# Performance work log

Measured on AMD Instinct MI355X. Metric: run time of the kernel, lower is better.

The kernel has to match this reference:

```python
import jax, jax.numpy as jnp
import numpy as np

_EPS = 1e-6
_ZCA_EPS = 1e-5
NEG_SLOPE_ATTN = 0.2   # LeakyReLU inside score_mlp
NEG_SLOPE_FFN = 0.1    # VNLinearLeakyReLU negative_slope


def _safe_norm(x, axis, keepdims=False):
    # norm with zero-gradient at exactly-zero vectors (matches torch subgradient)
    sq = jnp.sum(x * x, axis=axis, keepdims=keepdims)
    safe = jnp.where(sq == 0, 1.0, sq)
    return jnp.sqrt(safe) * (sq > 0)


def vn_linear(W, x):
    # W: (out, in); x: (B, C_in, 3, N) -> (B, C_out, 3, N)
    return jnp.einsum('oi,bivn->bovn', W, x)


def zca_layernorm(x, gamma):
    # x: (B, C, 3, N); whiten the 3D vector components per batch element
    B, C = x.shape[0], x.shape[1]
    xf = x.reshape(B, C, 3, -1).transpose(0, 2, 1, 3).reshape(B, 3, -1)
    xf = xf.astype(jnp.float32)
    mu = xf.mean(axis=-1, keepdims=True)
    xc = xf - mu
    M = xc.shape[-1]
    cov = (xc @ xc.transpose(0, 2, 1)) / (float(M) + _EPS)  # (B,3,3)
    cov = cov + _ZCA_EPS * jnp.eye(3, dtype=cov.dtype)[None]
    w, V = jnp.linalg.eigh(cov)
    w = jnp.maximum(w, _ZCA_EPS)
    Wm = (V * jax.lax.rsqrt(w)[:, None, :]) @ V.transpose(0, 2, 1)  # (B,3,3)
    xw = Wm @ xc
    xw = xw.reshape(B, 3, C, -1).transpose(0, 2, 1, 3).reshape(x.shape).astype(x.dtype)
    return xw * gamma[None, :, None, None]


def cwsa_attention(x, pos, Wq, Wk, Wv, Wo, W1, b1, W2, b2):
    q = vn_linear(Wq, x)  # (B,C,3,N)
    k = vn_linear(Wk, x)
    v = vn_linear(Wv, x)
    qk = q.transpose(0, 3, 1, 2)  # (B,N,C,3)
    kk = k.transpose(0, 3, 1, 2)
    vv = v.transpose(0, 3, 1, 2)
    rel = qk[:, :, None, :, :] - kk[:, None, :, :, :]      # (B,N,N,C,3)
    rel_norm = _safe_norm(rel, axis=-1)                    # (B,N,N,C)
    rel_mean = rel_norm.mean(axis=-1, keepdims=True)       # (B,N,N,1)
    rel_pos = pos[:, :, None, :] - pos[:, None, :, :]      # (B,N,N,3)
    rel_pos_norm = _safe_norm(rel_pos, axis=-1, keepdims=True)  # (B,N,N,1)
    score_in = jnp.concatenate([rel_mean, rel_pos_norm], axis=-1)  # (B,N,N,2)
    h = jax.nn.leaky_relu(score_in @ W1.T + b1, NEG_SLOPE_ATTN)
    scores = h @ W2.T + b2                                  # (B,N,N,C)
    attn = jax.nn.softmax(scores, axis=2)                   # softmax over keys j
    out = jnp.einsum('bijk,bjkd->bikd', attn, vv)           # (B,N,C,3)
    out = out.transpose(0, 2, 3, 1)                         # (B,C,3,N)
    return vn_linear(Wo, out)


def vn_leaky_relu(p, d, ns):
    # p, d: (B, C, 3, N)
    dot = jnp.sum(p * d, axis=2, keepdims=True)
    dsq = jnp.sum(d * d, axis=2, keepdims=True)
    mask = (dot >= 0).astype(p.dtype)
    proj = p - (dot / (dsq + _EPS)) * d
    return ns * p + (1.0 - ns) * (mask * p + (1.0 - mask) * proj)


def ffn(x, Wfeat, Wdir, Wffn2):
    p = vn_linear(Wfeat, x)
    d = vn_linear(Wdir, x)
    h = vn_leaky_relu(p, d, NEG_SLOPE_FFN)
    return vn_linear(Wffn2, h)


def setup_inputs() -> dict:
    key = jax.random.key(0)
    ks = jax.random.split(key, 16)
    B, C, N = 2, 128, 256
    hidden, ratio = 64, 2
    sC = 1.0 / np.sqrt(C)
    inp = {
        'x': jax.random.normal(ks[0], (B, C, 3, N), dtype=jnp.float32),
        'pos': jax.random.normal(ks[1], (B, N, 3), dtype=jnp.float32),
        'Wq': jax.random.normal(ks[2], (C, C), dtype=jnp.float32) * sC,
        'Wk': jax.random.normal(ks[3], (C, C), dtype=jnp.float32) * sC,
        'Wv': jax.random.normal(ks[4], (C, C), dtype=jnp.float32) * sC,
        'Wo': jax.random.normal(ks[5], (C, C), dtype=jnp.float32) * sC,
        'W1': jax.random.normal(ks[6], (hidden, 2), dtype=jnp.float32) * (1.0 / np.sqrt(2.0)),
        'b1': jnp.zeros((hidden,), dtype=jnp.float32),
        'W2': jax.random.normal(ks[7], (C, hidden), dtype=jnp.float32) * (1.0 / np.sqrt(hidden)),
        'b2': jnp.zeros((C,), dtype=jnp.float32),
        'gamma1': jnp.ones((C,), dtype=jnp.float32),
        'Wfeat': jax.random.normal(ks[8], (C * ratio, C), dtype=jnp.float32) * sC,
        'Wdir': jax.random.normal(ks[9], (C * ratio, C), dtype=jnp.float32) * sC,
        'Wffn2': jax.random.normal(ks[10], (C, C * ratio), dtype=jnp.float32) * (1.0 / np.sqrt(C * ratio)),
        'gamma2': jnp.ones((C,), dtype=jnp.float32),
    }
    return inp


def reference(x, pos, Wq, Wk, Wv, Wo, W1, b1, W2, b2, gamma1, Wfeat, Wdir, Wffn2, gamma2):
    a = cwsa_attention(x, pos, Wq, Wk, Wv, Wo, W1, b1, W2, b2)
    x1 = zca_layernorm(x + a, gamma1)
    f = ffn(x1, Wfeat, Wdir, Wffn2)
    return zca_layernorm(x1 + f, gamma2)
```

## Files before the change

### kernel.cpp

```cpp
#include <hip/hip_runtime.h>
#include <math.h>

#define BB 2
#define CC 128
#define NN 256
#define HH 64
#define CHX 256
#define COLS 768
#define NEG_ATTN 0.2f
#define NEG_FFN 0.1f

typedef __attribute__((ext_vector_type(8))) short short8b;
typedef __attribute__((ext_vector_type(4))) float f32x4;

__device__ __forceinline__ unsigned bf16rne(float x) {
  unsigned u = __float_as_uint(x);
  return (u + 0x7fffu + ((u >> 16) & 1u)) >> 16;
}

__global__ __launch_bounds__(256) void k_qkv(
    const float* __restrict__ x, const float* __restrict__ Wq,
    const float* __restrict__ Wk, const float* __restrict__ Wv,
    float* __restrict__ q_t, float* __restrict__ k_nat, float* __restrict__ v_t3)
{
  const int ct = blockIdx.x, which = blockIdx.y, b = blockIdx.z;
  const int col0 = ct * 16;
  __shared__ float xt[CC][16];
  const float* xb = x + (size_t)b * CC * COLS;
  for (int idx = threadIdx.x; idx < CC * 16; idx += 256) {
    int r = idx >> 4, cc = idx & 15;
    xt[r][cc] = xb[r * COLS + col0 + cc];
  }
  __syncthreads();
  const float* W = (which == 0) ? Wq : ((which == 1) ? Wk : Wv);
  const int co = threadIdx.x >> 1;
  const int cc0 = (threadIdx.x & 1) * 8;
  float acc[8];
#pragma unroll
  for (int k = 0; k < 8; k++) acc[k] = 0.f;
  const float* wrow = W + co * CC;
  for (int ci = 0; ci < CC; ci++) {
    float wv = wrow[ci];
#pragma unroll
    for (int k = 0; k < 8; k++) acc[k] = fmaf(wv, xt[ci][cc0 + k], acc[k]);
  }
#pragma unroll
  for (int k = 0; k < 8; k++) {
    int col = col0 + cc0 + k;
    int v = col >> 8, n = col & 255;
    float val = acc[k];
    if (which == 0)      q_t[((size_t)(b * NN + n) * CC + co) * 3 + v] = val;
    else if (which == 1) k_nat[(size_t)(b * CC + co) * COLS + col] = val;
    else                 v_t3[((size_t)(b * NN + n) * CC + co) * 3 + v] = val;
  }
}

__global__ __launch_bounds__(256) void k_rel(
    const float* __restrict__ q_t, const float* __restrict__ k_nat,
    const float* __restrict__ pos, float* __restrict__ rm_all,
    float* __restrict__ rp_all)
{
  const int i = blockIdx.x, b = blockIdx.y;
  const int t = threadIdx.x;
  __shared__ float qv[CC * 3];
  for (int idx = t; idx < CC * 3; idx += 256)
    qv[idx] = q_t[(size_t)(b * NN + i) * CC * 3 + idx];
  __syncthreads();
  const int j = t;
  const float* kb = k_nat + (size_t)b * CC * COLS;
  float p0 = 0.f, p1 = 0.f, p2 = 0.f, p3 = 0.f;
  for (int c = 0; c < CC; c += 4) {
    float kx0 = kb[(c + 0) * COLS + j], ky0 = kb[(c + 0) * COLS + 256 + j], kz0 = kb[(c + 0) * COLS + 512 + j];
    float kx1 = kb[(c + 1) * COLS + j], ky1 = kb[(c + 1) * COLS + 256 + j], kz1 = kb[(c + 1) * COLS + 512 + j];
    float kx2 = kb[(c + 2) * COLS + j], ky2 = kb[(c + 2) * COLS + 256 + j], kz2 = kb[(c + 2) * COLS + 512 + j];
    float kx3 = kb[(c + 3) * COLS + j], ky3 = kb[(c + 3) * COLS + 256 + j], kz3 = kb[(c + 3) * COLS + 512 + j];
    float dx, dy, dz, sq;
    dx = kx0 - qv[(c + 0) * 3]; dy = ky0 - qv[(c + 0) * 3 + 1]; dz = kz0 - qv[(c + 0) * 3 + 2];
    sq = dx * dx + dy * dy + dz * dz; p0 += (sq > 0.f) ? sqrtf(sq) : 0.f;
    dx = kx1 - qv[(c + 1) * 3]; dy = ky1 - qv[(c + 1) * 3 + 1]; dz = kz1 - qv[(c + 1) * 3 + 2];
    sq = dx * dx + dy * dy + dz * dz; p1 += (sq > 0.f) ? sqrtf(sq) : 0.f;
    dx = kx2 - qv[(c + 2) * 3]; dy = ky2 - qv[(c + 2) * 3 + 1]; dz = kz2 - qv[(c + 2) * 3 + 2];
    sq = dx * dx + dy * dy + dz * dz; p2 += (sq > 0.f) ? sqrtf(sq) : 0.f;
    dx = kx3 - qv[(c + 3) * 3]; dy = ky3 - qv[(c + 3) * 3 + 1]; dz = kz3 - qv[(c + 3) * 3 + 2];
    sq = dx * dx + dy * dy + dz * dz; p3 += (sq > 0.f) ? sqrtf(sq) : 0.f;
  }
  rm_all[(size_t)(b * NN + i) * NN + j] = ((p0 + p1) + (p2 + p3)) * (1.f / 128.f);
  float dx = pos[(b * NN + i) * 3 + 0] - pos[(b * NN + j) * 3 + 0];
  float dy = pos[(b * NN + i) * 3 + 1] - pos[(b * NN + j) * 3 + 1];
  float dz = pos[(b * NN + i) * 3 + 2] - pos[(b * NN + j) * 3 + 2];
  float sq = dx * dx + dy * dy + dz * dz;
  rp_all[(size_t)(b * NN + i) * NN + j] = (sq > 0.f) ? sqrtf(sq) : 0.f;
}

__global__ __launch_bounds__(256, 4) void k_attn(
    const float* __restrict__ rm_all, const float* __restrict__ rp_all,
    const float* __restrict__ v_t3, const float* __restrict__ W1,
    const float* __restrict__ b1, const float* __restrict__ W2,
    float* __restrict__ a_nat)
{
  const int i = blockIdx.x, chalf = blockIdx.y, b = blockIdx.z;
  const int t = threadIdx.x;
  __shared__ __align__(16) short hh_s[64 * 64];
  __shared__ __align__(16) short w2_s[64 * 64];
  __shared__ float sc_s[64 * 65];
  __shared__ float rm_s[NN], rp_s[NN];

  rm_s[t] = rm_all[(size_t)(b * NN + i) * NN + t];
  rp_s[t] = rp_all[(size_t)(b * NN + i) * NN + t];
  {
    const int cl = t >> 2, h0 = (t & 3) * 16;
    const float* wrow = W2 + (size_t)(chalf * 64 + cl) * HH + h0;
#pragma unroll
    for (int e = 0; e < 8; e++) {
      unsigned lo = bf16rne(wrow[2 * e]);
      unsigned hi = bf16rne(wrow[2 * e + 1]);
      int didx = (cl * 32 + (h0 >> 1) + e) ^ ((cl & 7) << 2);
      ((unsigned*)w2_s)[didx] = lo | (hi << 16);
    }
  }
  const int h2 = (t & 31) * 2, jgrp = t >> 5;
  const float4 w1v = *reinterpret_cast<const float4*>(W1 + 2 * h2);
  const float c0 = b1[h2], c1 = b1[h2 + 1];
  __syncthreads();

  auto phase2 = [&](int q) {
#pragma unroll
    for (int jj = 0; jj < 8; jj++) {
      int jl = jgrp * 8 + jj;
      int jg = q * 64 + jl;
      float rmv = rm_s[jg], rpv = rp_s[jg];
      float g0 = fmaf(w1v.x, rmv, fmaf(w1v.y, rpv, c0));
      float g1 = fmaf(w1v.z, rmv, fmaf(w1v.w, rpv, c1));
      g0 = (g0 >= 0.f) ? g0 : NEG_ATTN * g0;
      g1 = (g1 >= 0.f) ? g1 : NEG_ATTN * g1;
      int didx = (jl * 32 + (h2 >> 1)) ^ ((jl & 7) << 2);
      ((unsigned*)hh_s)[didx] = bf16rne(g0) | (bf16rne(g1) << 16);
    }
  };

  phase2(0);
  __syncthreads();

  const int lane = t & 63, wv = t >> 6;
  const int g8 = (lane >> 4) * 8;
  const int cdx = wv * 16 + (lane & 15);
  const short8b bfr0 = *reinterpret_cast<const short8b*>(&w2_s[(cdx * 64 + g8) ^ ((cdx & 7) << 3)]);
  const short8b bfr1 = *reinterpret_cast<const short8b*>(&w2_s[(cdx * 64 + 32 + g8) ^ ((cdx & 7) << 3)]);

  const int cl = lane;
  const int par = wv;
  const int vc = chalf * 64 + cl;
  float l = 0.f, a0 = 0.f, a1 = 0.f, a2 = 0.f;

  for (int q = 0; q < 4; q++) {
#pragma unroll
    for (int jt = 0; jt < 4; jt++) {
      int jr = jt * 16 + (lane & 15);
      short8b af0 = *reinterpret_cast<const short8b*>(&hh_s[(jr * 64 + g8) ^ ((jr & 7) << 3)]);
      short8b af1 = *reinterpret_cast<const short8b*>(&hh_s[(jr * 64 + 32 + g8) ^ ((jr & 7) << 3)]);
      f32x4 acc = {0.f, 0.f, 0.f, 0.f};
      acc = __builtin_amdgcn_mfma_f32_16x16x32_bf16(af0, bfr0, acc, 0, 0, 0);
      acc = __builtin_amdgcn_mfma_f32_16x16x32_bf16(af1, bfr1, acc, 0, 0, 0);
      int row0 = jt * 16 + (lane >> 4) * 4;
      int ccol = wv * 16 + (lane & 15);
#pragma unroll
      for (int r = 0; r < 4; r++) sc_s[(row0 + r) * 65 + ccol] = acc[r];
    }
    __syncthreads();
#pragma unroll 4
    for (int jj = 0; jj < 16; jj++) {
      int jl = jj * 4 + par;
      int jg = q * 64 + jl;
      float s = sc_s[jl * 65 + cl];
      const float* vb = v_t3 + ((size_t)(b * NN + jg) * CC + vc) * 3;
      float v0 = vb[0], v1 = vb[1], v2 = vb[2];
      float p = __expf(s);
      l += p;
      a0 = fmaf(p, v0, a0);
      a1 = fmaf(p, v1, a1);
      a2 = fmaf(p, v2, a2);
    }
    if (q < 3) phase2(q + 1);
    __syncthreads();
  }

  float* mrg = sc_s;
  if (par != 0) {
    float* mp = mrg + (cl * 3 + (par - 1)) * 4;
    mp[0] = l; mp[1] = a0; mp[2] = a1; mp[3] = a2;
  }
  __syncthreads();
  if (par == 0) {
    float L = l, A0 = a0, A1 = a1, A2 = a2;
#pragma unroll
    for (int q = 0; q < 3; q++) {
      const float* mp = mrg + (cl * 3 + q) * 4;
      L += mp[0]; A0 += mp[1]; A1 += mp[2]; A2 += mp[3];
    }
    float inv = 1.f / L;
    float* ap = a_nat + (size_t)(b * CC + vc) * COLS + i;
    ap[0] = A0 * inv; ap[256] = A1 * inv; ap[512] = A2 * inv;
  }
}

__global__ __launch_bounds__(256) void k_wo_res(
    const float* __restrict__ a_nat, const float* __restrict__ Wo,
    const float* __restrict__ x, float* __restrict__ y1)
{
  const int ct = blockIdx.x, cohalf = blockIdx.y, b = blockIdx.z;
  const int col0 = ct * 16;
  __shared__ float at[CC][16];
  const float* ab = a_nat + (size_t)b * CC * COLS;
  for (int idx = threadIdx.x; idx < CC * 16; idx += 256) {
    int r = idx >> 4, cc = idx & 15;
    at[r][cc] = ab[r * COLS + col0 + cc];
  }
  __syncthreads();
  const int co = cohalf * 64 + (threadIdx.x >> 2);
  const int cc0 = (threadIdx.x & 3) * 4;
  float acc[4];
#pragma unroll
  for (int k = 0; k < 4; k++) acc[k] = 0.f;
  const float* wrow = Wo + co * CC;
  for (int ci = 0; ci < CC; ci++) {
    float wv = wrow[ci];
#pragma unroll
    for (int k = 0; k < 4; k++) acc[k] = fmaf(wv, at[ci][cc0 + k], acc[k]);
  }
  const size_t base = (size_t)(b * CC + co) * COLS + col0 + cc0;
#pragma unroll
  for (int k = 0; k < 4; k++) y1[base + k] = x[base + k] + acc[k];
}

__global__ __launch_bounds__(1024) void k_stats(
    const float* __restrict__ y, float* __restrict__ stats)
{
  const int b = blockIdx.x;
  const float* yb = y + (size_t)b * CC * COLS;
  const int t = threadIdx.x;
  float v9[9];
#pragma unroll
  for (int k = 0; k < 9; k++) v9[k] = 0.f;
  for (int e = 0; e < 32; e++) {
    int idx = e * 1024 + t;
    int cidx = idx >> 8, n = idx & 255;
    const float* row = yb + cidx * COLS + n;
    float v0 = row[0], v1 = row[256], v2 = row[512];
    v9[0] += v0; v9[1] += v1; v9[2] += v2;
    v9[3] += v0 * v0; v9[4] += v0 * v1; v9[5] += v0 * v2;
    v9[6] += v1 * v1; v9[7] += v1 * v2; v9[8] += v2 * v2;
  }
#pragma unroll
  for (int off = 32; off >= 1; off >>= 1)
#pragma unroll
    for (int k = 0; k < 9; k++) v9[k] += __shfl_down(v9[k], off);
  __shared__ float red[16][9];
  const int wid = t >> 6, lane = t & 63;
  if (lane == 0)
#pragma unroll
    for (int k = 0; k < 9; k++) red[wid][k] = v9[k];
  __syncthreads();
  if (t == 0) {
    float tot[9];
#pragma unroll
    for (int k = 0; k < 9; k++) tot[k] = 0.f;
    for (int w = 0; w < 16; w++)
#pragma unroll
      for (int k = 0; k < 9; k++) tot[k] += red[w][k];
    const float M = (float)(CC * NN);
    float mu0 = tot[0] / M, mu1 = tot[1] / M, mu2 = tot[2] / M;
    float A[3][3];
    A[0][0] = (tot[3] - M * mu0 * mu0) / M + 1e-5f;
    A[0][1] = A[1][0] = (tot[4] - M * mu0 * mu1) / M;
    A[0][2] = A[2][0] = (tot[5] - M * mu0 * mu2) / M;
    A[1][1] = (tot[6] - M * mu1 * mu1) / M + 1e-5f;
    A[1][2] = A[2][1] = (tot[7] - M * mu1 * mu2) / M;
    A[2][2] = (tot[8] - M * mu2 * mu2) / M + 1e-5f;
    float V[3][3] = {{1.f, 0.f, 0.f}, {0.f, 1.f, 0.f}, {0.f, 0.f, 1.f}};
    for (int sweep = 0; sweep < 10; sweep++) {
      for (int pi = 0; pi < 3; pi++) {
        const int p = (pi == 2) ? 1 : 0;
        const int q = (pi == 0) ? 1 : 2;
        float apq = A[p][q];
        if (fabsf(apq) < 1e-30f) continue;
        float theta = (A[q][q] - A[p][p]) / (2.f * apq);
        float tt = 1.f / (fabsf(theta) + sqrtf(theta * theta + 1.f));
        if (theta < 0.f) tt = -tt;
        float cr = 1.f / sqrtf(tt * tt + 1.f);
        float sr = tt * cr;
        float app = A[p][p], aqq = A[q][q];
        A[p][p] = app - tt * apq;
        A[q][q] = aqq + tt * apq;
        A[p][q] = A[q][p] = 0.f;
        const int r = 3 - p - q;
        float arp = A[r][p], arq = A[r][q];
        A[r][p] = A[p][r] = cr * arp - sr * arq;
        A[r][q] = A[q][r] = sr * arp + cr * arq;
        for (int rr = 0; rr < 3; rr++) {
          float vrp = V[rr][p], vrq = V[rr][q];
          V[rr][p] = cr * vrp - sr * vrq;
          V[rr][q] = sr * vrp + cr * vrq;
        }
      }
    }
    float rs[3];
#pragma unroll
    for (int k = 0; k < 3; k++) rs[k] = rsqrtf(fmaxf(A[k][k], 1e-5f));
    float* st = stats + b * 12;
    st[0] = mu0; st[1] = mu1; st[2] = mu2;
    for (int u = 0; u < 3; u++)
      for (int v = 0; v < 3; v++) {
        float acc = 0.f;
        for (int k = 0; k < 3; k++) acc += V[u][k] * rs[k] * V[v][k];
        st[3 + u * 3 + v] = acc;
      }
  }
}

__global__ __launch_bounds__(256) void k_ffn1(
    const float* __restrict__ y1, const float* __restrict__ stats,
    const float* __restrict__ gamma, const float* __restrict__ Wfeat,
    const float* __restrict__ Wdir, float* __restrict__ hout)
{
  const int nt = blockIdx.x, cs = blockIdx.y, b = blockIdx.z;
  const int n0 = nt * 16, co0 = cs * 64;
  __shared__ float xt[CC][48];
  const float* yb = y1 + (size_t)b * CC * COLS;
  const float* st = stats + b * 12;
  for (int idx = threadIdx.x; idx < CC * 16; idx += 256) {
    int ci = idx >> 4, nn = idx & 15;
    const float* row = yb + ci * COLS + n0 + nn;
    float d0 = row[0] - st[0], d1 = row[256] - st[1], d2 = row[512] - st[2];
    float g = gamma[ci];
    xt[ci][nn]      = g * (st[3] * d0 + st[4] * d1 + st[5] * d2);
    xt[ci][16 + nn] = g * (st[6] * d0 + st[7] * d1 + st[8] * d2);
    xt[ci][32 + nn] = g * (st[9] * d0 + st[10] * d1 + st[11] * d2);
  }
  __syncthreads();
  const int co = co0 + (threadIdx.x & 63);
  const int nn0 = (threadIdx.x >> 6) * 4;
  float p[3][4], d[3][4];
#pragma unroll
  for (int v = 0; v < 3; v++)
#pragma unroll
    for (int k = 0; k < 4; k++) { p[v][k] = 0.f; d[v][k] = 0.f; }
  const float* wf = Wfeat + co * CC;
  const float* wd = Wdir + co * CC;
  for (int ci = 0; ci < CC; ci++) {
    float a = wf[ci], bb = wd[ci];
#pragma unroll
    for (int v = 0; v < 3; v++)
#pragma unroll
      for (int k = 0; k < 4; k++) {
        float xv = xt[ci][v * 16 + nn0 + k];
        p[v][k] = fmaf(a, xv, p[v][k]);
        d[v][k] = fmaf(bb, xv, d[v][k]);
      }
  }
  float* hb = hout + (size_t)(b * CHX + co) * COLS;
#pragma unroll
  for (int k = 0; k < 4; k++) {
    float dot = p[0][k] * d[0][k] + p[1][k] * d[1][k] + p[2][k] * d[2][k];
    float dsq = d[0][k] * d[0][k] + d[1][k] * d[1][k] + d[2][k] * d[2][k];
    float coef = (dot >= 0.f) ? 0.f : (1.f - NEG_FFN) * dot / (dsq + 1e-6f);
#pragma unroll
    for (int v = 0; v < 3; v++)
      hb[v * 256 + n0 + nn0 + k] = p[v][k] - coef * d[v][k];
  }
}

__global__ __launch_bounds__(256) void k_ffn2(
    const float* __restrict__ h, const float* __restrict__ Wffn2,
    const float* __restrict__ y1, const float* __restrict__ stats,
    const float* __restrict__ gamma, float* __restrict__ x2)
{
  const int ct = blockIdx.x, cohalf = blockIdx.y, b = blockIdx.z;
  const int col0 = ct * 16;
  __shared__ float ht[CHX][16];
  const float* hb = h + (size_t)b * CHX * COLS;
  for (int idx = threadIdx.x; idx < CHX * 16; idx += 256) {
    int r = idx >> 4, cc = idx & 15;
    ht[r][cc] = hb[r * COLS + col0 + cc];
  }
  __syncthreads();
  const int co = cohalf * 64 + (threadIdx.x >> 2);
  const int cc0 = (threadIdx.x & 3) * 4;
  float acc[4];
#pragma unroll
  for (int k = 0; k < 4; k++) acc[k] = 0.f;
  const float* w = Wffn2 + co * CHX;
  for (int ci = 0; ci < CHX; ci++) {
    float wv = w[ci];
#pragma unroll
    for (int k = 0; k < 4; k++) acc[k] = fmaf(wv, ht[ci][cc0 + k], acc[k]);
  }
  const int col_base = col0 + cc0;
  const int v = col_base >> 8, n = col_base & 255;
  const float* st = stats + b * 12;
  const float* yb = y1 + (size_t)(b * CC + co) * COLS + n;
  const float g = gamma[co];
  const float w0 = st[3 + v * 3 + 0], w1 = st[3 + v * 3 + 1], w2 = st[3 + v * 3 + 2];
  const size_t base = (size_t)(b * CC + co) * COLS + col_base;
#pragma unroll
  for (int k = 0; k < 4; k++) {
    float d0 = yb[k] - st[0], d1 = yb[256 + k] - st[1], d2 = yb[512 + k] - st[2];
    float xw = g * (w0 * d0 + w1 * d1 + w2 * d2);
    x2[base + k] = xw + acc[k];
  }
}

__global__ __launch_bounds__(256) void k_zca_apply(
    const float* __restrict__ y, const float* __restrict__ stats,
    const float* __restrict__ gamma, float* __restrict__ out)
{
  int idx = blockIdx.x * blockDim.x + threadIdx.x;
  int b = idx >> 15, rem = idx & 32767;
  int cidx = rem >> 8, n = rem & 255;
  const float* st = stats + b * 12;
  const size_t base = (size_t)(b * CC + cidx) * COLS + n;
  float v0 = y[base] - st[0];
  float v1 = y[base + 256] - st[1];
  float v2 = y[base + 512] - st[2];
  float g = gamma[cidx];
  out[base]       = g * (st[3] * v0 + st[4] * v1 + st[5] * v2);
  out[base + 256] = g * (st[6] * v0 + st[7] * v1 + st[8] * v2);
  out[base + 512] = g * (st[9] * v0 + st[10] * v1 + st[11] * v2);
}

extern "C" void kernel_launch(void* const* d_in, const int* in_sizes, int n_in,
                              void* d_out, int out_size, void* d_ws, size_t ws_size,
                              hipStream_t stream)
{
  (void)in_sizes; (void)n_in; (void)out_size; (void)ws_size;
  const float* x      = (const float*)d_in[0];
  const float* pos    = (const float*)d_in[1];
  const float* Wq     = (const float*)d_in[2];
  const float* Wk     = (const float*)d_in[3];
  const float* Wv     = (const float*)d_in[4];
  const float* Wo     = (const float*)d_in[5];
  const float* W1     = (const float*)d_in[6];
  const float* b1     = (const float*)d_in[7];
  const float* W2     = (const float*)d_in[8];
  const float* gamma1 = (const float*)d_in[10];
  const float* Wfeat  = (const float*)d_in[11];
  const float* Wdir   = (const float*)d_in[12];
  const float* Wffn2  = (const float*)d_in[13];
  const float* gamma2 = (const float*)d_in[14];

  float* ws = (float*)d_ws;
  const size_t SZ = (size_t)BB * CC * 3 * NN;
  const size_t RMSZ = (size_t)BB * NN * NN;
  float* q_t    = ws;
  float* k_nat  = ws + SZ;
  float* v_t3   = ws + 2 * SZ;
  float* rm_all = ws + 3 * SZ;
  float* rp_all = ws + 3 * SZ + RMSZ;
  float* a_nat  = ws;
  float* y1     = ws + SZ;
  float* hbuf   = ws + 2 * SZ;
  float* x2     = ws;
  float* stats1 = ws + 4 * SZ;
  float* stats2 = ws + 4 * SZ + 64;

  k_qkv<<<dim3(48, 3, BB), 256, 0, stream>>>(x, Wq, Wk, Wv, q_t, k_nat, v_t3);
  k_rel<<<dim3(NN, BB), 256, 0, stream>>>(q_t, k_nat, pos, rm_all, rp_all);
  k_attn<<<dim3(NN, 2, BB), 256, 0, stream>>>(rm_all, rp_all, v_t3, W1, b1, W2, a_nat);
  k_wo_res<<<dim3(48, 2, BB), 256, 0, stream>>>(a_nat, Wo, x, y1);
  k_stats<<<BB, 1024, 0, stream>>>(y1, stats1);
  k_ffn1<<<dim3(16, 4, BB), 256, 0, stream>>>(y1, stats1, gamma1, Wfeat, Wdir, hbuf);
  k_ffn2<<<dim3(48, 2, BB), 256, 0, stream>>>(hbuf, Wffn2, y1, stats1, gamma1, x2);
  k_stats<<<BB, 1024, 0, stream>>>(x2, stats2);
  k_zca_apply<<<256, 256, 0, stream>>>(x2, stats2, gamma2, (float*)d_out);
}
```

Before: 104.3 us.

## Split attention key range across blocks and merge partial softmax sums in Wo kernel

The attention kernel now splits the 256 keys into two halves handled by separate blocks, which doubles the grid. Each block writes unnormalized partial numerators and denominators, and the Wo/residual kernel sums the two halves and divides before the matmul. W2 fragments are now loaded straight from global memory into registers instead of being staged through shared memory, and the inner accumulation uses two interleaved accumulator sets to shorten dependency chains. This adds extra workspace traffic for the partial buffers and repeats the W2 conversion in every block.

Result: slower. 117.0 us (+12.1%).

```diff
diff --git a/kernel.cpp b/kernel.cpp
--- a/kernel.cpp
+++ b/kernel.cpp
@@ -96,39 +96,45 @@
     const float* __restrict__ rm_all, const float* __restrict__ rp_all,
     const float* __restrict__ v_t3, const float* __restrict__ W1,
     const float* __restrict__ b1, const float* __restrict__ W2,
-    float* __restrict__ a_nat)
-{
-  const int i = blockIdx.x, chalf = blockIdx.y, b = blockIdx.z;
+    float* __restrict__ a_p0, float* __restrict__ a_p1,
+    float* __restrict__ l_p0, float* __restrict__ l_p1)
+{
+  const int i = blockIdx.x, b = blockIdx.z;
+  const int chalf = blockIdx.y >> 1, qhalf = blockIdx.y & 1;
   const int t = threadIdx.x;
   __shared__ __align__(16) short hh_s[64 * 64];
-  __shared__ __align__(16) short w2_s[64 * 64];
   __shared__ float sc_s[64 * 65];
-  __shared__ float rm_s[NN], rp_s[NN];
-
-  rm_s[t] = rm_all[(size_t)(b * NN + i) * NN + t];
-  rp_s[t] = rp_all[(size_t)(b * NN + i) * NN + t];
-  {
-    const int cl = t >> 2, h0 = (t & 3) * 16;
-    const float* wrow = W2 + (size_t)(chalf * 64 + cl) * HH + h0;
-#pragma unroll
-    for (int e = 0; e < 8; e++) {
-      unsigned lo = bf16rne(wrow[2 * e]);
-      unsigned hi = bf16rne(wrow[2 * e + 1]);
-      int didx = (cl * 32 + (h0 >> 1) + e) ^ ((cl & 7) << 2);
-      ((unsigned*)w2_s)[didx] = lo | (hi << 16);
-    }
-  }
+  __shared__ float rm_s[128], rp_s[128];
+
+  if (t < 128) rm_s[t] = rm_all[(size_t)(b * NN + i) * NN + qhalf * 128 + t];
+  else         rp_s[t - 128] = rp_all[(size_t)(b * NN + i) * NN + qhalf * 128 + (t - 128)];
+
   const int h2 = (t & 31) * 2, jgrp = t >> 5;
   const float4 w1v = *reinterpret_cast<const float4*>(W1 + 2 * h2);
   const float c0 = b1[h2], c1 = b1[h2 + 1];
-  __syncthreads();
-
-  auto phase2 = [&](int q) {
+
+  const int lane = t & 63, wv = t >> 6;
+  const int g8 = (lane >> 4) * 8;
+  const int cdx = wv * 16 + (lane & 15);
+
+  const float* w2row = W2 + (size_t)(chalf * 64 + cdx) * HH;
+  const float4 wA = *reinterpret_cast<const float4*>(w2row + g8);
+  const float4 wB = *reinterpret_cast<const float4*>(w2row + g8 + 4);
+  const float4 wC = *reinterpret_cast<const float4*>(w2row + 32 + g8);
+  const float4 wD = *reinterpret_cast<const float4*>(w2row + 32 + g8 + 4);
+  uint4 u0 = { bf16rne(wA.x) | (bf16rne(wA.y) << 16), bf16rne(wA.z) | (bf16rne(wA.w) << 16),
+               bf16rne(wB.x) | (bf16rne(wB.y) << 16), bf16rne(wB.z) | (bf16rne(wB.w) << 16) };
+  uint4 u1 = { bf16rne(wC.x) | (bf16rne(wC.y) << 16), bf16rne(wC.z) | (bf16rne(wC.w) << 16),
+               bf16rne(wD.x) | (bf16rne(wD.y) << 16), bf16rne(wD.z) | (bf16rne(wD.w) << 16) };
+  const short8b bfr0 = __builtin_bit_cast(short8b, u0);
+  const short8b bfr1 = __builtin_bit_cast(short8b, u1);
+
+  auto phase2 = [&](int qq) {
 #pragma unroll
     for (int jj = 0; jj < 8; jj++) {
       int jl = jgrp * 8 + jj;
-      int jg = q * 64 + jl;
-      float rmv = rm_s[jg], rpv = rp_s[jg];
+      int jloc = qq * 64 + jl;
+      float rmv = rm_s[jloc], rpv = rp_s[jloc];
       float g0 = fmaf(w1v.x, rmv, fmaf(w1v.y, rpv, c0));
       float g1 = fmaf(w1v.z, rmv, fmaf(w1v.w, rpv, c1));
       g0 = (g0 >= 0.f) ? g0 : NEG_ATTN * g0;
@@ -138,21 +144,17 @@
     }
   };
 
+  __syncthreads();
   phase2(0);
   __syncthreads();
-
-  const int lane = t & 63, wv = t >> 6;
-  const int g8 = (lane >> 4) * 8;
-  const int cdx = wv * 16 + (lane & 15);
-  const short8b bfr0 = *reinterpret_cast<const short8b*>(&w2_s[(cdx * 64 + g8) ^ ((cdx & 7) << 3)]);
-  const short8b bfr1 = *reinterpret_cast<const short8b*>(&w2_s[(cdx * 64 + 32 + g8) ^ ((cdx & 7) << 3)]);
 
   const int cl = lane;
   const int par = wv;
   const int vc = chalf * 64 + cl;
-  float l = 0.f, a0 = 0.f, a1 = 0.f, a2 = 0.f;
-
-  for (int q = 0; q < 4; q++) {
+  float l[2] = {0.f, 0.f};
+  float a0[2] = {0.f, 0.f}, a1[2] = {0.f, 0.f}, a2[2] = {0.f, 0.f};
+
+  for (int qq = 0; qq < 2; qq++) {
 #pragma unroll
     for (int jt = 0; jt < 4; jt++) {
       int jr = jt * 16 + (lane & 15);
@@ -167,53 +169,62 @@
       for (int r = 0; r < 4; r++) sc_s[(row0 + r) * 65 + ccol] = acc[r];
     }
     __syncthreads();
-#pragma unroll 4
+    const int jbase = qhalf * 128 + qq * 64;
+#pragma unroll
     for (int jj = 0; jj < 16; jj++) {
       int jl = jj * 4 + par;
-      int jg = q * 64 + jl;
+      int jg = jbase + jl;
       float s = sc_s[jl * 65 + cl];
       const float* vb = v_t3 + ((size_t)(b * NN + jg) * CC + vc) * 3;
-      float v0 = vb[0], v1 = vb[1], v2 = vb[2];
       float p = __expf(s);
-      l += p;
-      a0 = fmaf(p, v0, a0);
-      a1 = fmaf(p, v1, a1);
-      a2 = fmaf(p, v2, a2);
+      int ch = jj & 1;
+      l[ch] += p;
+      a0[ch] = fmaf(p, vb[0], a0[ch]);
+      a1[ch] = fmaf(p, vb[1], a1[ch]);
+      a2[ch] = fmaf(p, vb[2], a2[ch]);
     }
-    if (q < 3) phase2(q + 1);
+    if (qq == 0) phase2(1);
     __syncthreads();
   }
+
+  float L = l[0] + l[1], A0 = a0[0] + a0[1], A1 = a1[0] + a1[1], A2 = a2[0] + a2[1];
 
   float* mrg = sc_s;
   if (par != 0) {
     float* mp = mrg + (cl * 3 + (par - 1)) * 4;
-    mp[0] = l; mp[1] = a0; mp[2] = a1; mp[3] = a2;
+    mp[0] = L; mp[1] = A0; mp[2] = A1; mp[3] = A2;
   }
   __syncthreads();
   if (par == 0) {
-    float L = l, A0 = a0, A1 = a1, A2 = a2;
 #pragma unroll
     for (int q = 0; q < 3; q++) {
       const float* mp = mrg + (cl * 3 + q) * 4;
       L += mp[0]; A0 += mp[1]; A1 += mp[2]; A2 += mp[3];
     }
-    float inv = 1.f / L;
-    float* ap = a_nat + (size_t)(b * CC + vc) * COLS + i;
-    ap[0] = A0 * inv; ap[256] = A1 * inv; ap[512] = A2 * inv;
+    float* lp = (qhalf == 0) ? l_p0 : l_p1;
+    float* ap = ((qhalf == 0) ? a_p0 : a_p1) + (size_t)(b * CC + vc) * COLS + i;
+    lp[(size_t)(b * CC + vc) * NN + i] = L;
+    ap[0] = A0; ap[256] = A1; ap[512] = A2;
   }
 }
 
 __global__ __launch_bounds__(256) void k_wo_res(
-    const float* __restrict__ a_nat, const float* __restrict__ Wo,
-    const float* __restrict__ x, float* __restrict__ y1)
+    const float* __restrict__ a_p0, const float* __restrict__ a_p1,
+    const float* __restrict__ l_p0, const float* __restrict__ l_p1,
+    const float* __restrict__ Wo, const float* __restrict__ x,
+    float* __restrict__ y1)
 {
   const int ct = blockIdx.x, cohalf = blockIdx.y, b = blockIdx.z;
   const int col0 = ct * 16;
+  const int n0 = col0 & 255;
   __shared__ float at[CC][16];
-  const float* ab = a_nat + (size_t)b * CC * COLS;
+  const size_t abase = (size_t)b * CC * COLS;
+  const size_t lbase = (size_t)b * CC * NN;
   for (int idx = threadIdx.x; idx < CC * 16; idx += 256) {
     int r = idx >> 4, cc = idx & 15;
-    at[r][cc] = ab[r * COLS + col0 + cc];
+    float L = l_p0[lbase + r * NN + n0 + cc] + l_p1[lbase + r * NN + n0 + cc];
+    float A = a_p0[abase + r * COLS + col0 + cc] + a_p1[abase + r * COLS + col0 + cc];
+    at[r][cc] = A / L;
   }
   __syncthreads();
   const int co = cohalf * 64 + (threadIdx.x >> 2);
@@ -448,24 +459,31 @@
   const float* gamma2 = (const float*)d_in[14];
 
   float* ws = (float*)d_ws;
-  const size_t SZ = (size_t)BB * CC * 3 * NN;
-  const size_t RMSZ = (size_t)BB * NN * NN;
+  const size_t QKV = (size_t)BB * NN * CC * 3;
+  const size_t RM  = (size_t)BB * NN * NN;
+  const size_t LP  = (size_t)BB * CC * NN;
+  const size_t HB  = (size_t)BB * CHX * COLS;
+
   float* q_t    = ws;
-  float* k_nat  = ws + SZ;
-  float* v_t3   = ws + 2 * SZ;
-  float* rm_all = ws + 3 * SZ;
-  float* rp_all = ws + 3 * SZ + RMSZ;
-  float* a_nat  = ws;
-  float* y1     = ws + SZ;
-  float* hbuf   = ws + 2 * SZ;
-  float* x2     = ws;
-  float* stats1 = ws + 4 * SZ;
-  float* stats2 = ws + 4 * SZ + 64;
+  float* k_nat  = q_t    + QKV;
+  float* v_t3   = k_nat  + QKV;
+  float* rm_all = v_t3   + QKV;
+  float* rp_all = rm_all + RM;
+  float* a_p0   = rp_all + RM;
+  float* a_p1   = a_p0   + QKV;
+  float* l_p0   = a_p1   + QKV;
+  float* l_p1   = l_p0   + LP;
+  float* y1     = l_p1   + LP;
+  float* hbuf   = y1     + QKV;
+  float* x2     = hbuf   + HB;
+  float* stats1 = x2     + QKV;
+  float* stats2 = stats1 + 64;
 
   k_qkv<<<dim3(48, 3, BB), 256, 0, stream>>>(x, Wq, Wk, Wv, q_t, k_nat, v_t3);
   k_rel<<<dim3(NN, BB), 256, 0, stream>>>(q_t, k_nat, pos, rm_all, rp_all);
-  k_attn<<<dim3(NN, 2, BB), 256, 0, stream>>>(rm_all, rp_all, v_t3, W1, b1, W2, a_nat);
-  k_wo_res<<<dim3(48, 2, BB), 256, 0, stream>>>(a_nat, Wo, x, y1);
+  k_attn<<<dim3(NN, 4, BB), 256, 0, stream>>>(rm_all, rp_all, v_t3, W1, b1, W2,
+                                              a_p0, a_p1, l_p0, l_p1);
+  k_wo_res<<<dim3(48, 2, BB), 256, 0, stream>>>(a_p0, a_p1, l_p0, l_p1, Wo, x, y1);
   k_stats<<<BB, 1024, 0, stream>>>(y1, stats1);
   k_ffn1<<<dim3(16, 4, BB), 256, 0, stream>>>(y1, stats1, gamma1, Wfeat, Wdir, hbuf);
   k_ffn2<<<dim3(48, 2, BB), 256, 0, stream>>>(hbuf, Wffn2, y1, stats1, gamma1, x2);
```
